# Kernel tuning notes

Measured on AMD Instinct MI355X. Metric: run time of the kernel, lower is better.

Reference implementation:

```python
import jax, jax.numpy as jnp
import numpy as np


def _lin(x, w, b=None):
    # torch nn.Linear convention: y = x @ W^T + b, W: (out, in)
    y = jnp.einsum('...d,ed->...e', x, w)
    return y + b if b is not None else y


def setup_inputs() -> dict:
    key = jax.random.key(0)
    B, N, M, d = 8, 256, 128, 128
    ks = jax.random.split(key, 20)
    sc = 1.0 / np.sqrt(d)
    inp = {
        's': jax.random.normal(ks[0], (B, N, d), jnp.float32),
        'v': jax.random.normal(ks[1], (B, N, M, d), jnp.float32),
        'gs': jax.random.normal(ks[2], (B, d), jnp.float32),
        'gv': jax.random.normal(ks[3], (B, M, d), jnp.float32),
        'gv2': jax.random.normal(ks[4], (B, M, M, d), jnp.float32),
        'lin1_w': jax.random.normal(ks[5], (d, d), jnp.float32) * sc,
        'lin1_b': jax.random.normal(ks[6], (d,), jnp.float32) * sc,
        'lin2_w': jax.random.normal(ks[7], (d, d), jnp.float32) * sc,
        'lin2_b': jax.random.normal(ks[8], (d,), jnp.float32) * sc,
        'lin3_w': jax.random.normal(ks[9], (d, d), jnp.float32) * sc,
        'lin3_b': jax.random.normal(ks[10], (d,), jnp.float32) * sc,
        'linv1_w': jax.random.normal(ks[11], (d, d), jnp.float32) * sc,
        'linv2_w': jax.random.normal(ks[12], (d, d), jnp.float32) * sc,
        'linv3_w': jax.random.normal(ks[13], (d, d), jnp.float32) * sc,
        'mlp_w1': jax.random.normal(ks[14], (d, d), jnp.float32) * sc,
        'mlp_b1': jax.random.normal(ks[15], (d,), jnp.float32) * sc,
        'mlp_w2': jax.random.normal(ks[16], (d, d), jnp.float32) * sc,
        'mlp_b2': jax.random.normal(ks[17], (d,), jnp.float32) * sc,
    }
    return inp


def reference(s, v, gs, gv, gv2,
              lin1_w, lin1_b, lin2_w, lin2_b, lin3_w, lin3_b,
              linv1_w, linv2_w, linv3_w,
              mlp_w1, mlp_b1, mlp_w2, mlp_b2):
    # v update: three (B,N,M,d) branches, averaged
    v_vv2 = _lin(jnp.einsum('bnmd,bmcd->bncd', v, gv2), linv1_w)
    v_vs = _lin(gs[:, None, None, :] * v, linv3_w)
    v_sv = _lin(s[:, :, None, :] * gv[:, None, :, :], linv2_w)
    v_new = (v_vv2 + v_sv + v_vs) / 3
    # s update
    s_v2t = jnp.einsum('bmmd->bd', gv2)                 # per-channel trace of gv2
    s_vv = jnp.einsum('bmd,bnmd->bnd', gv, v_new)
    s_new = ((_lin(s_v2t, lin1_w, lin1_b) * gs)[:, None, :]
             * _lin(s, lin2_w, lin2_b)
             * _lin(s_vv, lin3_w, lin3_b))
    # MLP: Linear -> ReLU -> Linear
    s_new = _lin(jax.nn.relu(_lin(s_new, mlp_w1, mlp_b1)), mlp_w2, mlp_b2)
    return (s_new, v_new)
```

## Files before the change

kernel.cpp:

```cpp
#include <hip/hip_runtime.h>
#include <hip/hip_bf16.h>
#include <stdint.h>

#define B_ 8
#define N_ 256
#define M_ 128
#define D_ 128

typedef __attribute__((ext_vector_type(8))) short short8;
typedef __attribute__((ext_vector_type(4))) short short4v;
typedef __attribute__((ext_vector_type(4))) float f32x4;

static __device__ __forceinline__ unsigned short f2bf(float x) {
    union { float f; unsigned int u; } c; c.f = x;
    unsigned int r = (c.u + 0x7FFFu + ((c.u >> 16) & 1u)) >> 16;
    return (unsigned short)r;
}
static __device__ __forceinline__ unsigned short bfhu(float x) {
    union { float f; unsigned int u; } c; c.f = x;
    return (unsigned short)((c.u + 0x8000u) >> 16);
}
static __device__ __forceinline__ unsigned int pkhu(float a, float b) {
    union { float f; unsigned int u; } ca, cb; ca.f = a; cb.f = b;
    unsigned int ua = ca.u + 0x8000u;
    unsigned int ub = cb.u + 0x8000u;
    return (ua >> 16) | (ub & 0xFFFF0000u);
}
static __device__ __forceinline__ float4 mul4(float4 a, float4 b) {
    return make_float4(a.x * b.x, a.y * b.y, a.z * b.z, a.w * b.w);
}
static __device__ __forceinline__ short8 pack8(float4 a, float4 b) {
    return (short8){(short)f2bf(a.x), (short)f2bf(a.y), (short)f2bf(a.z), (short)f2bf(a.w),
                    (short)f2bf(b.x), (short)f2bf(b.y), (short)f2bf(b.z), (short)f2bf(b.w)};
}

__global__ void k0a_prep(const float* __restrict__ lin2_w, const float* __restrict__ lin3_w,
                         const float* __restrict__ mlp_w1, const float* __restrict__ mlp_w2,
                         const float* __restrict__ linv1_w, const float* __restrict__ linv2_w,
                         const float* __restrict__ linv3_w,
                         float* __restrict__ wT2, float* __restrict__ wT3,
                         float* __restrict__ wTm1, float* __restrict__ wTm2,
                         unsigned short* __restrict__ wfrag) {
    int gid = blockIdx.x * 256 + threadIdx.x;
    int task = gid >> 14;
    int idx = gid & 16383;
    if (task < 4) {
        int e = idx & 127, dd = idx >> 7;
        const float* src = task == 0 ? lin2_w : task == 1 ? lin3_w : task == 2 ? mlp_w1 : mlp_w2;
        float* dst = task == 0 ? wT2 : task == 1 ? wT3 : task == 2 ? wTm1 : wTm2;
        dst[dd * 128 + e] = src[e * 128 + dd];
    } else {
        int mat = task - 4;
        const float* src = mat == 0 ? linv1_w : mat == 1 ? linv2_w : linv3_w;
        int e = idx >> 7, k = idx & 127;
        int dst = ((((e >> 4) * 12 + (mat * 4 + (k >> 5))) * 4 + ((k >> 3) & 3)) * 16 + (e & 15)) * 8
                  + (k & 7);
        wfrag[dst] = f2bf(src[idx] * (1.0f / 3.0f));
    }
}

__global__ void k0b_trace(const float* __restrict__ gv2, float* __restrict__ s_v2t) {
    int b = blockIdx.x, d = threadIdx.x;
    const float* p = gv2 + (size_t)b * (M_ * M_ * D_) + d;
    float acc = 0.f;
    #pragma unroll 8
    for (int m = 0; m < 128; ++m) acc += p[(size_t)m * 16512];
    s_v2t[b * 128 + d] = acc;
}

__global__ void k0c_g1(const float* __restrict__ s_v2t, const float* __restrict__ lin1_w,
                       const float* __restrict__ lin1_b, const float* __restrict__ gs,
                       float* __restrict__ g1) {
    __shared__ float sv[128];
    int b = blockIdx.x, e = threadIdx.x;
    sv[e] = s_v2t[b * 128 + e];
    __syncthreads();
    const float* w = lin1_w + e * 128;
    float acc = 0.f;
    #pragma unroll 4
    for (int dd = 0; dd < 128; ++dd) acc = fmaf(sv[dd], w[dd], acc);
    g1[b * 128 + e] = (acc + lin1_b[e]) * gs[b * 128 + e];
}

__global__ __launch_bounds__(512, 4) void k1_T2(const float* __restrict__ v,
                                                const float* __restrict__ gv2,
                                                unsigned short* __restrict__ t2base) {
    __shared__ unsigned short sm[40960];
    int bid = blockIdx.x;
    int b = bid & 7;
    int r = bid >> 3;
    int dc = r & 15;
    int ch = (r >> 4) & 1;
    int nt = r >> 5;
    int n0 = nt * 64, c0 = ch * 64, d0 = dc * 8;
    int t = threadIdx.x;
    int w = t >> 6, lane = t & 63, ln15 = lane & 15, kg = lane >> 4;

    f32x4 acc[4][4];
    #pragma unroll
    for (int i = 0; i < 4; ++i)
        #pragma unroll
        for (int j = 0; j < 4; ++j) acc[i][j] = (f32x4){0.f, 0.f, 0.f, 0.f};

    int mgA = t & 7, nA = t >> 3;
    int mgB = t & 7, cB = t >> 3;

    for (int mc = 0; mc < 4; ++mc) {
        int m0 = mc * 32;
        {
            const float* src = v + ((size_t)(b * N_ + n0 + nA) * M_ + (m0 + mgA * 4)) * D_ + d0;
            float4 x[4][2];
            #pragma unroll
            for (int mi = 0; mi < 4; ++mi) {
                x[mi][0] = *(const float4*)(src + mi * 128);
                x[mi][1] = *(const float4*)(src + mi * 128 + 4);
            }
            unsigned short* bse = &sm[nA * 40 + mgA * 4];
            #pragma unroll
            for (int dh = 0; dh < 2; ++dh) {
                uint2 p0 = make_uint2(pkhu(x[0][dh].x, x[1][dh].x), pkhu(x[2][dh].x, x[3][dh].x));
                uint2 p1 = make_uint2(pkhu(x[0][dh].y, x[1][dh].y), pkhu(x[2][dh].y, x[3][dh].y));
                uint2 p2 = make_uint2(pkhu(x[0][dh].z, x[1][dh].z), pkhu(x[2][dh].z, x[3][dh].z));
                uint2 p3 = make_uint2(pkhu(x[0][dh].w, x[1][dh].w), pkhu(x[2][dh].w, x[3][dh].w));
                *(uint2*)(bse + (dh * 4 + 0) * 2560) = p0;
                *(uint2*)(bse + (dh * 4 + 1) * 2560) = p1;
                *(uint2*)(bse + (dh * 4 + 2) * 2560) = p2;
                *(uint2*)(bse + (dh * 4 + 3) * 2560) = p3;
            }
        }
        {
            const float* src = gv2 + ((size_t)(b * M_ + m0 + mgB * 4) * M_ + (c0 + cB)) * D_ + d0;
            float4 x[4][2];
            #pragma unroll
            for (int mi = 0; mi < 4; ++mi) {
                x[mi][0] = *(const float4*)(src + (size_t)mi * 16384);
                x[mi][1] = *(const float4*)(src + (size_t)mi * 16384 + 4);
            }
            unsigned short* bse = &sm[20480 + cB * 40 + mgB * 4];
            #pragma unroll
            for (int dh = 0; dh < 2; ++dh) {
                uint2 p0 = make_uint2(pkhu(x[0][dh].x, x[1][dh].x), pkhu(x[2][dh].x, x[3][dh].x));
                uint2 p1 = make_uint2(pkhu(x[0][dh].y, x[1][dh].y), pkhu(x[2][dh].y, x[3][dh].y));
                uint2 p2 = make_uint2(pkhu(x[0][dh].z, x[1][dh].z), pkhu(x[2][dh].z, x[3][dh].z));
                uint2 p3 = make_uint2(pkhu(x[0][dh].w, x[1][dh].w), pkhu(x[2][dh].w, x[3][dh].w));
                *(uint2*)(bse + (dh * 4 + 0) * 2560) = p0;
                *(uint2*)(bse + (dh * 4 + 1) * 2560) = p1;
                *(uint2*)(bse + (dh * 4 + 2) * 2560) = p2;
                *(uint2*)(bse + (dh * 4 + 3) * 2560) = p3;
            }
        }
        __syncthreads();
        short8 af[4], bf[4];
        #pragma unroll
        for (int i = 0; i < 4; ++i)
            af[i] = *(const short8*)&sm[w * 2560 + (i * 16 + ln15) * 40 + kg * 8];
        #pragma unroll
        for (int j = 0; j < 4; ++j)
            bf[j] = *(const short8*)&sm[20480 + w * 2560 + (j * 16 + ln15) * 40 + kg * 8];
        #pragma unroll
        for (int i = 0; i < 4; ++i)
            #pragma unroll
            for (int j = 0; j < 4; ++j)
                acc[i][j] = __builtin_amdgcn_mfma_f32_16x16x32_bf16(af[i], bf[j], acc[i][j], 0, 0, 0);
        __syncthreads();
    }
    #pragma unroll
    for (int i = 0; i < 4; ++i)
        #pragma unroll
        for (int j = 0; j < 4; ++j)
            #pragma unroll
            for (int q = 0; q < 4; ++q) {
                int n = i * 16 + kg * 4 + q;
                int c = j * 16 + ln15;
                sm[n * 520 + c * 8 + w] = bfhu(acc[i][j][q]);
            }
    __syncthreads();
    #pragma unroll
    for (int p = 0; p < 8; ++p) {
        int u = p * 512 + t;
        int n = u >> 6;
        int c = u & 63;
        short8 x = *(const short8*)&sm[n * 520 + c * 8];
        size_t kb = (size_t)(b * N_ + n0 + n) * 2 + ch;
        *(short8*)(t2base + kb * 16384 + (size_t)((c >> 4) * 16 + dc) * 128 + (c & 15) * 8) = x;
    }
}

__global__ __launch_bounds__(512, 2) void k2_vnew(
        const float* __restrict__ s, const float* __restrict__ v,
        const float* __restrict__ gs, const float* __restrict__ gv,
        const unsigned short* __restrict__ wfrag,
        float* __restrict__ vnew, float* __restrict__ svv) {
    __shared__ unsigned short smw[49152];
    __shared__ float part[2][4][128];
    int t = threadIdx.x;
    int w = t >> 6;
    int sb = w >> 2;
    int w4 = w & 3;
    int kb2 = blockIdx.x * 2 + sb;
    int b = kb2 >> 8;
    int lane = t & 63, ln15 = lane & 15, kgrp = lane >> 4;

    #pragma unroll
    for (int r = 0; r < 12; ++r) {
        int idx = (r * 512 + t) * 8;
        *(short8*)&smw[idx] = *(const short8*)(wfrag + idx);
    }
    const unsigned short* t2u = (const unsigned short*)(vnew + (size_t)kb2 * 16384);
    short8 aT[2][4];
    #pragma unroll
    for (int h = 0; h < 2; ++h) {
        int rt = w4 * 2 + h;
        const unsigned short* tb = t2u + (rt >> 2) * 16384 + ((rt & 3) * 16 + kgrp) * 128 + ln15 * 8;
        #pragma unroll
        for (int kk = 0; kk < 4; ++kk)
            aT[h][kk] = *(const short8*)(tb + kk * 512);
    }
    const float* srow = s + (size_t)kb2 * 128;
    const float* gsr  = gs + (size_t)b * 128;
    float4 ss[8], qq[8];
    #pragma unroll
    for (int kk = 0; kk < 4; ++kk) {
        int dd = kk * 32 + kgrp * 8;
        ss[kk * 2]     = *(const float4*)(srow + dd);
        ss[kk * 2 + 1] = *(const float4*)(srow + dd + 4);
        qq[kk * 2]     = *(const float4*)(gsr + dd);
        qq[kk * 2 + 1] = *(const float4*)(gsr + dd + 4);
    }
    __syncthreads();

    float psum[8] = {0.f, 0.f, 0.f, 0.f, 0.f, 0.f, 0.f, 0.f};
    #pragma unroll
    for (int h = 0; h < 2; ++h) {
        int rt = w4 * 2 + h;
        int ca = rt * 16 + ln15;
        const float* gvr = gv + ((size_t)b * M_ + ca) * D_;
        const float* vr  = v + ((size_t)kb2 * M_ + ca) * D_;
        short8 aD[8];
        #pragma unroll
        for (int kk = 0; kk < 4; ++kk) {
            int dd = kk * 32 + kgrp * 8;
            float4 g0 = *(const float4*)(gvr + dd), g1 = *(const float4*)(gvr + dd + 4);
            float4 v0 = *(const float4*)(vr + dd),  v1 = *(const float4*)(vr + dd + 4);
            aD[kk]     = pack8(mul4(ss[kk * 2], g0), mul4(ss[kk * 2 + 1], g1));
            aD[4 + kk] = pack8(mul4(qq[kk * 2], v0), mul4(qq[kk * 2 + 1], v1));
        }
        float* outp = vnew + (size_t)kb2 * 16384 + (rt >> 2) * 8192;
        int rowl = (rt & 3) * 16 + kgrp * 4;
        const float* grow = gv + ((size_t)b * M_ + rt * 16 + kgrp * 4) * D_;
        #pragma unroll
        for (int ct = 0; ct < 8; ++ct) {
            f32x4 acc = {0.f, 0.f, 0.f, 0.f};
            #pragma unroll
            for (int kk = 0; kk < 12; ++kk) {
                short8 a = (kk < 4) ? aT[h][kk] : aD[kk - 4];
                short8 bfr = *(const short8*)&smw[(((ct * 12 + kk) * 4 + kgrp) * 16 + ln15) * 8];
                acc = __builtin_amdgcn_mfma_f32_16x16x32_bf16(a, bfr, acc, 0, 0, 0);
            }
            int e = ct * 16 + ln15;
            #pragma unroll
            for (int q = 0; q < 4; ++q) {
                outp[(size_t)(rowl + q) * 128 + e] = acc[q];
                psum[ct] = fmaf(grow[(size_t)q * 128 + e], acc[q], psum[ct]);
            }
        }
    }
    #pragma unroll
    for (int ct = 0; ct < 8; ++ct) {
        psum[ct] += __shfl_xor(psum[ct], 16);
        psum[ct] += __shfl_xor(psum[ct], 32);
    }
    if (kgrp == 0) {
        #pragma unroll
        for (int ct = 0; ct < 8; ++ct) part[sb][w4][ct * 16 + ln15] = psum[ct];
    }
    __syncthreads();
    int tl = t & 255;
    int sb2 = t >> 8;
    if (tl < 128) {
        int kbo = blockIdx.x * 2 + sb2;
        svv[(size_t)kbo * 128 + tl] =
            part[sb2][0][tl] + part[sb2][1][tl] + part[sb2][2][tl] + part[sb2][3][tl];
    }
}

__global__ __launch_bounds__(256) void k4_spath(
        const float* __restrict__ s, const float* __restrict__ svv,
        const float* __restrict__ g1,
        const float* __restrict__ wT2, const float* __restrict__ lin2_b,
        const float* __restrict__ wT3, const float* __restrict__ lin3_b,
        const float* __restrict__ wTm1, const float* __restrict__ mlp_b1,
        const float* __restrict__ wTm2, const float* __restrict__ mlp_b2,
        float* __restrict__ sout) {
    __shared__ float xs[8][128], xv[8][128], pre[8][128], hbuf[8][128];
    int t = threadIdx.x;
    int rowb = blockIdx.x * 8;
    int b = rowb >> 8;
    #pragma unroll
    for (int i = 0; i < 4; ++i) {
        int vi = i * 256 + t;
        int r = vi >> 7, dd = vi & 127;
        xs[r][dd] = s[(size_t)(rowb + r) * 128 + dd];
        xv[r][dd] = svv[(size_t)(rowb + r) * 128 + dd];
    }
    __syncthreads();
    int e = t & 127, h2 = t >> 7;
    float b2 = lin2_b[e], b3 = lin3_b[e], g1v = g1[b * 128 + e];
    float a2[4] = {b2, b2, b2, b2}, a3[4] = {b3, b3, b3, b3};
    for (int dd = 0; dd < 128; ++dd) {
        float w2 = wT2[dd * 128 + e], w3 = wT3[dd * 128 + e];
        #pragma unroll
        for (int r = 0; r < 4; ++r) {
            a2[r] = fmaf(xs[h2 * 4 + r][dd], w2, a2[r]);
            a3[r] = fmaf(xv[h2 * 4 + r][dd], w3, a3[r]);
        }
    }
    #pragma unroll
    for (int r = 0; r < 4; ++r) pre[h2 * 4 + r][e] = g1v * a2[r] * a3[r];
    __syncthreads();
    float bm1 = mlp_b1[e];
    float ah[4] = {bm1, bm1, bm1, bm1};
    for (int dd = 0; dd < 128; ++dd) {
        float w = wTm1[dd * 128 + e];
        #pragma unroll
        for (int r = 0; r < 4; ++r) ah[r] = fmaf(pre[h2 * 4 + r][dd], w, ah[r]);
    }
    #pragma unroll
    for (int r = 0; r < 4; ++r) hbuf[h2 * 4 + r][e] = fmaxf(ah[r], 0.f);
    __syncthreads();
    float bm2 = mlp_b2[e];
    float ao[4] = {bm2, bm2, bm2, bm2};
    for (int dd = 0; dd < 128; ++dd) {
        float w = wTm2[dd * 128 + e];
        #pragma unroll
        for (int r = 0; r < 4; ++r) ao[r] = fmaf(hbuf[h2 * 4 + r][dd], w, ao[r]);
    }
    #pragma unroll
    for (int r = 0; r < 4; ++r) sout[(size_t)(rowb + h2 * 4 + r) * 128 + e] = ao[r];
}

extern "C" void kernel_launch(void* const* d_in, const int* in_sizes, int n_in,
                              void* d_out, int out_size, void* d_ws, size_t ws_size,
                              hipStream_t stream) {
    const float* s       = (const float*)d_in[0];
    const float* v       = (const float*)d_in[1];
    const float* gs      = (const float*)d_in[2];
    const float* gv      = (const float*)d_in[3];
    const float* gv2     = (const float*)d_in[4];
    const float* lin1_w  = (const float*)d_in[5];
    const float* lin1_b  = (const float*)d_in[6];
    const float* lin2_w  = (const float*)d_in[7];
    const float* lin2_b  = (const float*)d_in[8];
    const float* lin3_w  = (const float*)d_in[9];
    const float* lin3_b  = (const float*)d_in[10];
    const float* linv1_w = (const float*)d_in[11];
    const float* linv2_w = (const float*)d_in[12];
    const float* linv3_w = (const float*)d_in[13];
    const float* mlp_w1  = (const float*)d_in[14];
    const float* mlp_b1  = (const float*)d_in[15];
    const float* mlp_w2  = (const float*)d_in[16];
    const float* mlp_b2  = (const float*)d_in[17];

    float* sout = (float*)d_out;
    float* vnew = (float*)d_out + 262144;

    float* wsf   = (float*)d_ws;
    float* wT2   = wsf;
    float* wT3   = wsf + 16384;
    float* wTm1  = wsf + 32768;
    float* wTm2  = wsf + 49152;
    float* s_v2t = wsf + 65536;
    float* g1    = wsf + 66560;
    float* svv   = wsf + 67584;
    unsigned short* wfrag = (unsigned short*)(wsf + 329728);

    k0a_prep<<<448, 256, 0, stream>>>(lin2_w, lin3_w, mlp_w1, mlp_w2,
                                      linv1_w, linv2_w, linv3_w,
                                      wT2, wT3, wTm1, wTm2, wfrag);
    k0b_trace<<<8, 128, 0, stream>>>(gv2, s_v2t);
    k0c_g1<<<8, 128, 0, stream>>>(s_v2t, lin1_w, lin1_b, gs, g1);
    k1_T2<<<1024, 512, 0, stream>>>(v, gv2, (unsigned short*)vnew);
    k2_vnew<<<1024, 512, 0, stream>>>(s, v, gs, gv, wfrag, vnew, svv);
    k4_spath<<<256, 256, 0, stream>>>(s, svv, g1, wT2, lin2_b, wT3, lin3_b,
                                      wTm1, mlp_b1, wTm2, mlp_b2, sout);
}
```

Baseline: 290.1 us.

## Retile k1_T2 to 32x32 n/c tiles over 32 channels with swizzled LDS

Restructures the per-channel batched GEMM kernel. Each block now covers 32 n by 32 c over 32 d-channels instead of 64x64 over 8 channels, and each wave owns 4 channels. Staging now does coalesced float4 loads along d into an XOR-swizzled LDS layout, and the output transpose uses a swizzled scatter. Shared memory grows to about 144KB with launch bounds of one block per CU, which cuts occupancy and latency hiding in exchange for wider contiguous global reads.

```diff
diff --git a/kernel.cpp b/kernel.cpp
--- a/kernel.cpp
+++ b/kernel.cpp
@@ -19,12 +19,6 @@
 static __device__ __forceinline__ unsigned short bfhu(float x) {
     union { float f; unsigned int u; } c; c.f = x;
     return (unsigned short)((c.u + 0x8000u) >> 16);
-}
-static __device__ __forceinline__ unsigned int pkhu(float a, float b) {
-    union { float f; unsigned int u; } ca, cb; ca.f = a; cb.f = b;
-    unsigned int ua = ca.u + 0x8000u;
-    unsigned int ub = cb.u + 0x8000u;
-    return (ua >> 16) | (ub & 0xFFFF0000u);
 }
 static __device__ __forceinline__ float4 mul4(float4 a, float4 b) {
     return make_float4(a.x * b.x, a.y * b.y, a.z * b.z, a.w * b.w);
@@ -82,107 +76,110 @@
     g1[b * 128 + e] = (acc + lin1_b[e]) * gs[b * 128 + e];
 }
 
-__global__ __launch_bounds__(512, 4) void k1_T2(const float* __restrict__ v,
+__global__ __launch_bounds__(512, 1) void k1_T2(const float* __restrict__ v,
                                                 const float* __restrict__ gv2,
                                                 unsigned short* __restrict__ t2base) {
-    __shared__ unsigned short sm[40960];
+    __shared__ __attribute__((aligned(16))) unsigned short sm[73728];
     int bid = blockIdx.x;
     int b = bid & 7;
     int r = bid >> 3;
-    int dc = r & 15;
-    int ch = (r >> 4) & 1;
-    int nt = r >> 5;
-    int n0 = nt * 64, c0 = ch * 64, d0 = dc * 8;
+    int ct = r & 3, dq = (r >> 2) & 3, nt = r >> 4;
+    int n0 = nt * 32, c0 = ct * 32, d0 = dq * 32;
     int t = threadIdx.x;
-    int w = t >> 6, lane = t & 63, ln15 = lane & 15, kg = lane >> 4;
-
-    f32x4 acc[4][4];
-    #pragma unroll
-    for (int i = 0; i < 4; ++i)
-        #pragma unroll
-        for (int j = 0; j < 4; ++j) acc[i][j] = (f32x4){0.f, 0.f, 0.f, 0.f};
-
-    int mgA = t & 7, nA = t >> 3;
-    int mgB = t & 7, cB = t >> 3;
+    int w = t >> 6, lane = t & 63, ln15 = lane & 15, kgrp = lane >> 4;
+    int f = t & 7;
+    int g = t >> 3;
+    int fsw = (f & 3) << 2;
+    int frw = f >> 2;
+
+    f32x4 acc[4][2][2];
+    #pragma unroll
+    for (int p = 0; p < 4; ++p)
+        #pragma unroll
+        for (int i2 = 0; i2 < 2; ++i2)
+            #pragma unroll
+            for (int j2 = 0; j2 < 2; ++j2) acc[p][i2][j2] = (f32x4){0.f, 0.f, 0.f, 0.f};
 
     for (int mc = 0; mc < 4; ++mc) {
         int m0 = mc * 32;
-        {
-            const float* src = v + ((size_t)(b * N_ + n0 + nA) * M_ + (m0 + mgA * 4)) * D_ + d0;
-            float4 x[4][2];
-            #pragma unroll
-            for (int mi = 0; mi < 4; ++mi) {
-                x[mi][0] = *(const float4*)(src + mi * 128);
-                x[mi][1] = *(const float4*)(src + mi * 128 + 4);
+        #pragma unroll
+        for (int i = 0; i < 16; ++i) {
+            int L = i * 64 + g;
+            int na = L >> 5, ma = L & 31;
+            float4 x = *(const float4*)(v + (((size_t)(b * N_ + n0 + na) * M_) + m0 + ma) * D_
+                                          + d0 + f * 4);
+            int mp = ma ^ fsw;
+            int np = na ^ frw;
+            #pragma unroll
+            for (int j = 0; j < 4; ++j)
+                sm[(f * 4 + j) * 1152 + np * 36 + mp] = bfhu(((const float*)&x)[j]);
+        }
+        #pragma unroll
+        for (int i = 0; i < 16; ++i) {
+            int L = i * 64 + g;
+            int ma = L >> 5, ca = L & 31;
+            float4 x = *(const float4*)(gv2 + (((size_t)(b * M_ + m0 + ma) * M_) + c0 + ca) * D_
+                                           + d0 + f * 4);
+            int mp = ma ^ fsw;
+            int cp = ca ^ frw;
+            #pragma unroll
+            for (int j = 0; j < 4; ++j)
+                sm[36864 + (f * 4 + j) * 1152 + cp * 36 + mp] = bfhu(((const float*)&x)[j]);
+        }
+        __syncthreads();
+        #pragma unroll
+        for (int p = 0; p < 4; ++p) {
+            int d = w * 4 + p;
+            int dbA = d * 1152, dbB = 36864 + d * 1152;
+            int sw = w & 3, nsw = (w >> 2) & 1;
+            int g0 = ((kgrp * 2) ^ sw) * 4, g1 = ((kgrp * 2 + 1) ^ sw) * 4;
+            short8 aF[2], bF[2];
+            #pragma unroll
+            for (int u2 = 0; u2 < 2; ++u2) {
+                int row = ((u2 * 16 + ln15) ^ nsw) * 36;
+                short4v lo = *(const short4v*)&sm[dbA + row + g0];
+                short4v hi = *(const short4v*)&sm[dbA + row + g1];
+                aF[u2] = __builtin_shufflevector(lo, hi, 0, 1, 2, 3, 4, 5, 6, 7);
+                short4v lo2 = *(const short4v*)&sm[dbB + row + g0];
+                short4v hi2 = *(const short4v*)&sm[dbB + row + g1];
+                bF[u2] = __builtin_shufflevector(lo2, hi2, 0, 1, 2, 3, 4, 5, 6, 7);
             }
-            unsigned short* bse = &sm[nA * 40 + mgA * 4];
-            #pragma unroll
-            for (int dh = 0; dh < 2; ++dh) {
-                uint2 p0 = make_uint2(pkhu(x[0][dh].x, x[1][dh].x), pkhu(x[2][dh].x, x[3][dh].x));
-                uint2 p1 = make_uint2(pkhu(x[0][dh].y, x[1][dh].y), pkhu(x[2][dh].y, x[3][dh].y));
-                uint2 p2 = make_uint2(pkhu(x[0][dh].z, x[1][dh].z), pkhu(x[2][dh].z, x[3][dh].z));
-                uint2 p3 = make_uint2(pkhu(x[0][dh].w, x[1][dh].w), pkhu(x[2][dh].w, x[3][dh].w));
-                *(uint2*)(bse + (dh * 4 + 0) * 2560) = p0;
-                *(uint2*)(bse + (dh * 4 + 1) * 2560) = p1;
-                *(uint2*)(bse + (dh * 4 + 2) * 2560) = p2;
-                *(uint2*)(bse + (dh * 4 + 3) * 2560) = p3;
-            }
-        }
-        {
-            const float* src = gv2 + ((size_t)(b * M_ + m0 + mgB * 4) * M_ + (c0 + cB)) * D_ + d0;
-            float4 x[4][2];
-            #pragma unroll
-            for (int mi = 0; mi < 4; ++mi) {
-                x[mi][0] = *(const float4*)(src + (size_t)mi * 16384);
-                x[mi][1] = *(const float4*)(src + (size_t)mi * 16384 + 4);
-            }
-            unsigned short* bse = &sm[20480 + cB * 40 + mgB * 4];
-            #pragma unroll
-            for (int dh = 0; dh < 2; ++dh) {
-                uint2 p0 = make_uint2(pkhu(x[0][dh].x, x[1][dh].x), pkhu(x[2][dh].x, x[3][dh].x));
-                uint2 p1 = make_uint2(pkhu(x[0][dh].y, x[1][dh].y), pkhu(x[2][dh].y, x[3][dh].y));
-                uint2 p2 = make_uint2(pkhu(x[0][dh].z, x[1][dh].z), pkhu(x[2][dh].z, x[3][dh].z));
-                uint2 p3 = make_uint2(pkhu(x[0][dh].w, x[1][dh].w), pkhu(x[2][dh].w, x[3][dh].w));
-                *(uint2*)(bse + (dh * 4 + 0) * 2560) = p0;
-                *(uint2*)(bse + (dh * 4 + 1) * 2560) = p1;
-                *(uint2*)(bse + (dh * 4 + 2) * 2560) = p2;
-                *(uint2*)(bse + (dh * 4 + 3) * 2560) = p3;
-            }
+            #pragma unroll
+            for (int i2 = 0; i2 < 2; ++i2)
+                #pragma unroll
+                for (int j2 = 0; j2 < 2; ++j2)
+                    acc[p][i2][j2] = __builtin_amdgcn_mfma_f32_16x16x32_bf16(
+                        aF[i2], bF[j2], acc[p][i2][j2], 0, 0, 0);
         }
         __syncthreads();
-        short8 af[4], bf[4];
-        #pragma unroll
-        for (int i = 0; i < 4; ++i)
-            af[i] = *(const short8*)&sm[w * 2560 + (i * 16 + ln15) * 40 + kg * 8];
-        #pragma unroll
-        for (int j = 0; j < 4; ++j)
-            bf[j] = *(const short8*)&sm[20480 + w * 2560 + (j * 16 + ln15) * 40 + kg * 8];
-        #pragma unroll
-        for (int i = 0; i < 4; ++i)
-            #pragma unroll
-            for (int j = 0; j < 4; ++j)
-                acc[i][j] = __builtin_amdgcn_mfma_f32_16x16x32_bf16(af[i], bf[j], acc[i][j], 0, 0, 0);
-        __syncthreads();
-    }
-    #pragma unroll
-    for (int i = 0; i < 4; ++i)
-        #pragma unroll
-        for (int j = 0; j < 4; ++j)
-            #pragma unroll
-            for (int q = 0; q < 4; ++q) {
-                int n = i * 16 + kg * 4 + q;
-                int c = j * 16 + ln15;
-                sm[n * 520 + c * 8 + w] = bfhu(acc[i][j][q]);
-            }
-    __syncthreads();
-    #pragma unroll
-    for (int p = 0; p < 8; ++p) {
-        int u = p * 512 + t;
-        int n = u >> 6;
-        int c = u & 63;
-        short8 x = *(const short8*)&sm[n * 520 + c * 8];
-        size_t kb = (size_t)(b * N_ + n0 + n) * 2 + ch;
-        *(short8*)(t2base + kb * 16384 + (size_t)((c >> 4) * 16 + dc) * 128 + (c & 15) * 8) = x;
+    }
+    #pragma unroll
+    for (int p = 0; p < 4; ++p) {
+        int d = w * 4 + p;
+        #pragma unroll
+        for (int i2 = 0; i2 < 2; ++i2)
+            #pragma unroll
+            for (int j2 = 0; j2 < 2; ++j2)
+                #pragma unroll
+                for (int q = 0; q < 4; ++q) {
+                    int n = i2 * 16 + kgrp * 4 + q;
+                    int c = j2 * 16 + ln15;
+                    int X = ((n >> 2) & 3) ^ (c & 3);
+                    sm[(n * 32 + c) * 40 + (d ^ (X << 3))] = bfhu(acc[p][i2][j2][q]);
+                }
+    }
+    __syncthreads();
+    #pragma unroll
+    for (int i = 0; i < 8; ++i) {
+        int u = i * 512 + t;
+        int n = u >> 7, c = (u >> 2) & 31, oct = u & 3;
+        int X = ((n >> 2) & 3) ^ (c & 3);
+        short8 x = *(const short8*)&sm[(n * 32 + c) * 40 + ((oct ^ X) << 3)];
+        int cg = c0 + c;
+        int octg = dq * 4 + oct;
+        size_t idx = ((size_t)((b * N_ + n0 + n) * 2 + (cg >> 6))) * 16384
+                   + (size_t)((cg >> 4) & 3) * 2048 + (size_t)octg * 128 + (cg & 15) * 8;
+        *(short8*)(t2base + idx) = x;
     }
 }
 
```

Result: slower. 394.5 us (+36.0%).

## Pre-transpose v and gv2 to bf16 d-major layouts before the T2 GEMM

Applied to the files above, without the earlier changes.

Adds two transpose kernels that convert v and gv2 from fp32 into bf16 buffers with d as the outer dimension, using XOR-swizzled shared-memory tiles. The T2 MFMA kernel then loads contiguous short8 vectors instead of strided fp32 gathers with in-register packing, and its block index order is changed. This aims to cut the scattered, poorly coalesced loads in the main GEMM, at the cost of an extra full pass that reads v and gv2 and writes about 80 MB of workspace. A legacy fallback path, with a different load scheme, is kept for when the workspace is too small.

```diff
diff --git a/kernel.cpp b/kernel.cpp
--- a/kernel.cpp
+++ b/kernel.cpp
@@ -22,9 +22,7 @@
 }
 static __device__ __forceinline__ unsigned int pkhu(float a, float b) {
     union { float f; unsigned int u; } ca, cb; ca.f = a; cb.f = b;
-    unsigned int ua = ca.u + 0x8000u;
-    unsigned int ub = cb.u + 0x8000u;
-    return (ua >> 16) | (ub & 0xFFFF0000u);
+    return ((ca.u + 0x8000u) >> 16) | ((cb.u + 0x8000u) & 0xFFFF0000u);
 }
 static __device__ __forceinline__ float4 mul4(float4 a, float4 b) {
     return make_float4(a.x * b.x, a.y * b.y, a.z * b.z, a.w * b.w);
@@ -82,16 +80,72 @@
     g1[b * 128 + e] = (acc + lin1_b[e]) * gs[b * 128 + e];
 }
 
-__global__ __launch_bounds__(512, 4) void k1_T2(const float* __restrict__ v,
-                                                const float* __restrict__ gv2,
-                                                unsigned short* __restrict__ t2base) {
+__global__ __launch_bounds__(256) void kt_v(const float* __restrict__ v,
+                                            unsigned short* __restrict__ vT) {
+    __shared__ unsigned short tl[128 * 136];
+    int bid = blockIdx.x;
+    int b = bid >> 8;
+    int R0 = (bid & 255) * 128;
+    int t = threadIdx.x;
+    const float* src = v + ((size_t)b * 32768 + R0) * 128;
+    #pragma unroll
+    for (int i = 0; i < 16; ++i) {
+        int flat = i * 256 + t;
+        int row = flat >> 5, slot = flat & 31;
+        float4 x = *(const float4*)(src + (size_t)row * 128 + slot * 4);
+        #pragma unroll
+        for (int j = 0; j < 4; ++j) {
+            int d = slot * 4 + j;
+            tl[d * 136 + (row ^ (((d >> 2) & 7) << 3))] = bfhu(((const float*)&x)[j]);
+        }
+    }
+    __syncthreads();
+    #pragma unroll
+    for (int i = 0; i < 8; ++i) {
+        int flat = i * 256 + t;
+        int d = flat >> 4, rs = flat & 15;
+        short8 y = *(const short8*)&tl[d * 136 + ((rs * 8) ^ (((d >> 2) & 7) << 3))];
+        *(short8*)(vT + (size_t)(b * 128 + d) * 32768 + R0 + rs * 8) = y;
+    }
+}
+
+__global__ __launch_bounds__(256) void kt_g(const float* __restrict__ gv2,
+                                            unsigned short* __restrict__ gT) {
+    __shared__ unsigned short tl[128 * 136];
+    int bid = blockIdx.x;
+    int b = bid >> 7;
+    int c = bid & 127;
+    int t = threadIdx.x;
+    const float* src = gv2 + ((size_t)(b * 128) * 128 + c) * 128;
+    #pragma unroll
+    for (int i = 0; i < 16; ++i) {
+        int flat = i * 256 + t;
+        int m = flat >> 5, slot = flat & 31;
+        float4 x = *(const float4*)(src + (size_t)m * 16384 + slot * 4);
+        #pragma unroll
+        for (int j = 0; j < 4; ++j) {
+            int d = slot * 4 + j;
+            tl[d * 136 + (m ^ (((d >> 2) & 7) << 3))] = bfhu(((const float*)&x)[j]);
+        }
+    }
+    __syncthreads();
+    #pragma unroll
+    for (int i = 0; i < 8; ++i) {
+        int flat = i * 256 + t;
+        int d = flat >> 4, ms = flat & 15;
+        short8 y = *(const short8*)&tl[d * 136 + ((ms * 8) ^ (((d >> 2) & 7) << 3))];
+        *(short8*)(gT + ((size_t)(b * 128 + d) * 128 + c) * 128 + ms * 8) = y;
+    }
+}
+
+__global__ __launch_bounds__(512, 2) void k1_T2_fast(const unsigned short* __restrict__ vT,
+                                                     const unsigned short* __restrict__ gT,
+                                                     unsigned short* __restrict__ t2base) {
     __shared__ unsigned short sm[40960];
     int bid = blockIdx.x;
     int b = bid & 7;
     int r = bid >> 3;
-    int dc = r & 15;
-    int ch = (r >> 4) & 1;
-    int nt = r >> 5;
+    int nt = r & 3, ch = (r >> 2) & 1, dc = r >> 3;
     int n0 = nt * 64, c0 = ch * 64, d0 = dc * 8;
     int t = threadIdx.x;
     int w = t >> 6, lane = t & 63, ln15 = lane & 15, kg = lane >> 4;
@@ -101,53 +155,19 @@
     for (int i = 0; i < 4; ++i)
         #pragma unroll
         for (int j = 0; j < 4; ++j) acc[i][j] = (f32x4){0.f, 0.f, 0.f, 0.f};
-
-    int mgA = t & 7, nA = t >> 3;
-    int mgB = t & 7, cB = t >> 3;
 
     for (int mc = 0; mc < 4; ++mc) {
         int m0 = mc * 32;
-        {
-            const float* src = v + ((size_t)(b * N_ + n0 + nA) * M_ + (m0 + mgA * 4)) * D_ + d0;
-            float4 x[4][2];
-            #pragma unroll
-            for (int mi = 0; mi < 4; ++mi) {
-                x[mi][0] = *(const float4*)(src + mi * 128);
-                x[mi][1] = *(const float4*)(src + mi * 128 + 4);
-            }
-            unsigned short* bse = &sm[nA * 40 + mgA * 4];
-            #pragma unroll
-            for (int dh = 0; dh < 2; ++dh) {
-                uint2 p0 = make_uint2(pkhu(x[0][dh].x, x[1][dh].x), pkhu(x[2][dh].x, x[3][dh].x));
-                uint2 p1 = make_uint2(pkhu(x[0][dh].y, x[1][dh].y), pkhu(x[2][dh].y, x[3][dh].y));
-                uint2 p2 = make_uint2(pkhu(x[0][dh].z, x[1][dh].z), pkhu(x[2][dh].z, x[3][dh].z));
-                uint2 p3 = make_uint2(pkhu(x[0][dh].w, x[1][dh].w), pkhu(x[2][dh].w, x[3][dh].w));
-                *(uint2*)(bse + (dh * 4 + 0) * 2560) = p0;
-                *(uint2*)(bse + (dh * 4 + 1) * 2560) = p1;
-                *(uint2*)(bse + (dh * 4 + 2) * 2560) = p2;
-                *(uint2*)(bse + (dh * 4 + 3) * 2560) = p3;
-            }
-        }
-        {
-            const float* src = gv2 + ((size_t)(b * M_ + m0 + mgB * 4) * M_ + (c0 + cB)) * D_ + d0;
-            float4 x[4][2];
-            #pragma unroll
-            for (int mi = 0; mi < 4; ++mi) {
-                x[mi][0] = *(const float4*)(src + (size_t)mi * 16384);
-                x[mi][1] = *(const float4*)(src + (size_t)mi * 16384 + 4);
-            }
-            unsigned short* bse = &sm[20480 + cB * 40 + mgB * 4];
-            #pragma unroll
-            for (int dh = 0; dh < 2; ++dh) {
-                uint2 p0 = make_uint2(pkhu(x[0][dh].x, x[1][dh].x), pkhu(x[2][dh].x, x[3][dh].x));
-                uint2 p1 = make_uint2(pkhu(x[0][dh].y, x[1][dh].y), pkhu(x[2][dh].y, x[3][dh].y));
-                uint2 p2 = make_uint2(pkhu(x[0][dh].z, x[1][dh].z), pkhu(x[2][dh].z, x[3][dh].z));
-                uint2 p3 = make_uint2(pkhu(x[0][dh].w, x[1][dh].w), pkhu(x[2][dh].w, x[3][dh].w));
-                *(uint2*)(bse + (dh * 4 + 0) * 2560) = p0;
-                *(uint2*)(bse + (dh * 4 + 1) * 2560) = p1;
-                *(uint2*)(bse + (dh * 4 + 2) * 2560) = p2;
-                *(uint2*)(bse + (dh * 4 + 3) * 2560) = p3;
-            }
+        #pragma unroll
+        for (int i = 0; i < 4; ++i) {
+            int flat = i * 512 + t;
+            int d = flat >> 8, x = (flat >> 2) & 63, ms = flat & 3;
+            short8 a = *(const short8*)(vT + ((size_t)(b * 128 + d0 + d) * 256 + n0 + x) * 128
+                                           + m0 + ms * 8);
+            *(short8*)&sm[d * 2560 + x * 40 + ms * 8] = a;
+            short8 g = *(const short8*)(gT + ((size_t)(b * 128 + d0 + d) * 128 + c0 + x) * 128
+                                           + m0 + ms * 8);
+            *(short8*)&sm[20480 + d * 2560 + x * 40 + ms * 8] = g;
         }
         __syncthreads();
         short8 af[4], bf[4];
@@ -181,6 +201,89 @@
         int n = u >> 6;
         int c = u & 63;
         short8 x = *(const short8*)&sm[n * 520 + c * 8];
+        size_t kb = (size_t)(b * N_ + n0 + n) * 2 + ch;
+        *(short8*)(t2base + kb * 16384 + (size_t)((c >> 4) * 16 + dc) * 128 + (c & 15) * 8) = x;
+    }
+}
+
+__global__ __launch_bounds__(512, 4) void k1_T2_legacy(const float* __restrict__ v,
+                                                       const float* __restrict__ gv2,
+                                                       unsigned short* __restrict__ t2base) {
+    __shared__ unsigned short sm[40960];
+    int bid = blockIdx.x;
+    int b = bid & 7;
+    int r = bid >> 3;
+    int nt = r & 3, ch = (r >> 2) & 1, dc = r >> 3;
+    int n0 = nt * 64, c0 = ch * 64, d0 = dc * 8;
+    int t = threadIdx.x;
+    int w = t >> 6, lane = t & 63, ln15 = lane & 15, kg = lane >> 4;
+
+    f32x4 acc[4][4];
+    #pragma unroll
+    for (int i = 0; i < 4; ++i)
+        #pragma unroll
+        for (int j = 0; j < 4; ++j) acc[i][j] = (f32x4){0.f, 0.f, 0.f, 0.f};
+
+    int d0l = (t & 1) * 4;
+    int am = (t >> 1) & 31, anb = t >> 6;
+    int bc = (t >> 1) & 63, bmb = t >> 7;
+
+    for (int mc = 0; mc < 4; ++mc) {
+        int m0 = mc * 32;
+        {
+            const float* src = v + (((size_t)(b * N_ + n0) * M_ + m0 + am) * D_ + d0 + d0l);
+            #pragma unroll
+            for (int p = 0; p < 8; ++p) {
+                int n = p * 8 + anb;
+                float4 x = *(const float4*)(src + (size_t)n * (M_ * D_));
+                #pragma unroll
+                for (int j = 0; j < 4; ++j)
+                    sm[(d0l + j) * 2560 + n * 40 + am] = f2bf(((const float*)&x)[j]);
+            }
+        }
+        {
+            const float* src = gv2 + (((size_t)(b * M_ + m0) * M_ + c0 + bc) * D_ + d0 + d0l);
+            #pragma unroll
+            for (int p = 0; p < 8; ++p) {
+                int m = p * 4 + bmb;
+                float4 x = *(const float4*)(src + (size_t)m * (M_ * D_));
+                #pragma unroll
+                for (int j = 0; j < 4; ++j)
+                    sm[20480 + (d0l + j) * 2560 + bc * 40 + m] = f2bf(((const float*)&x)[j]);
+            }
+        }
+        __syncthreads();
+        short8 af[4], bf[4];
+        #pragma unroll
+        for (int i = 0; i < 4; ++i)
+            af[i] = *(const short8*)&sm[w * 2560 + (i * 16 + ln15) * 40 + kg * 8];
+        #pragma unroll
+        for (int j = 0; j < 4; ++j)
+            bf[j] = *(const short8*)&sm[20480 + w * 2560 + (j * 16 + ln15) * 40 + kg * 8];
+        #pragma unroll
+        for (int i = 0; i < 4; ++i)
+            #pragma unroll
+            for (int j = 0; j < 4; ++j)
+                acc[i][j] = __builtin_amdgcn_mfma_f32_16x16x32_bf16(af[i], bf[j], acc[i][j], 0, 0, 0);
+        __syncthreads();
+    }
+    #pragma unroll
+    for (int i = 0; i < 4; ++i)
+        #pragma unroll
+        for (int j = 0; j < 4; ++j)
+            #pragma unroll
+            for (int q = 0; q < 4; ++q) {
+                int n = i * 16 + kg * 4 + q;
+                int c = j * 16 + ln15;
+                sm[(n * 64 + c) * 8 + w] = f2bf(acc[i][j][q]);
+            }
+    __syncthreads();
+    #pragma unroll
+    for (int p = 0; p < 8; ++p) {
+        int u = p * 512 + t;
+        int n = u >> 6;
+        int c = u & 63;
+        short8 x = *(const short8*)&sm[(n * 64 + c) * 8];
         size_t kb = (size_t)(b * N_ + n0 + n) * 2 + ch;
         *(short8*)(t2base + kb * 16384 + (size_t)((c >> 4) * 16 + dc) * 128 + (c & 15) * 8) = x;
     }
@@ -373,13 +476,22 @@
     float* g1    = wsf + 66560;
     float* svv   = wsf + 67584;
     unsigned short* wfrag = (unsigned short*)(wsf + 329728);
+    unsigned short* vT = (unsigned short*)((char*)d_ws + 2097152);
+    unsigned short* gT = (unsigned short*)((char*)d_ws + 69206016);
+    bool big = ws_size >= 102760448ULL;
 
     k0a_prep<<<448, 256, 0, stream>>>(lin2_w, lin3_w, mlp_w1, mlp_w2,
                                       linv1_w, linv2_w, linv3_w,
                                       wT2, wT3, wTm1, wTm2, wfrag);
     k0b_trace<<<8, 128, 0, stream>>>(gv2, s_v2t);
     k0c_g1<<<8, 128, 0, stream>>>(s_v2t, lin1_w, lin1_b, gs, g1);
-    k1_T2<<<1024, 512, 0, stream>>>(v, gv2, (unsigned short*)vnew);
+    if (big) {
+        kt_v<<<2048, 256, 0, stream>>>(v, vT);
+        kt_g<<<1024, 256, 0, stream>>>(gv2, gT);
+        k1_T2_fast<<<1024, 512, 0, stream>>>(vT, gT, (unsigned short*)vnew);
+    } else {
+        k1_T2_legacy<<<1024, 512, 0, stream>>>(v, gv2, (unsigned short*)vnew);
+    }
     k2_vnew<<<1024, 512, 0, stream>>>(s, v, gs, gv, wfrag, vnew, svv);
     k4_spath<<<256, 256, 0, stream>>>(s, svv, g1, wT2, lin2_b, wT3, lin3_b,
                                       wTm1, mlp_b1, wTm2, mlp_b2, sout);
```

New measurement: 263.2 us. 9.3% less time.
